# Optimization experiments

Measured on AMD Instinct MI355X. Metric: run time of the kernel, lower is better.

## Reference

```python
import jax, jax.numpy as jnp
import numpy as np

N_NODES = 100000
EMB = 256
HID = 64
N_REL = 5
N_EDGES = 3200000
BATCH = 16384


def _rgcn_conv(x, W, root, b, src, dst, etype):
    # PyG RGCNConv with mean aggregation per relation:
    # out_i = sum_r mean_{j in N_r(i)} x_j @ W_r + x_i @ root + b
    N = x.shape[0]
    R = W.shape[0]
    h = jnp.einsum('ni,rio->rno', x, W)          # [R, N, O] per-relation transforms
    m = h[etype, src]                            # [E, O] per-edge messages
    seg = dst * R + etype                        # combined (node, relation) segment id
    sums = jax.ops.segment_sum(m, seg, num_segments=N * R)
    cnt = jax.ops.segment_sum(jnp.ones((m.shape[0],), dtype=x.dtype), seg,
                              num_segments=N * R)
    mean = sums / jnp.maximum(cnt, 1.0)[:, None]
    agg = mean.reshape(N, R, -1).sum(axis=1)     # sum over relations
    return agg + x @ root + b


def _merge(x1, x2, w1, b1, w2, b2):
    x = jnp.concatenate([x1, x2], axis=1)
    h = jax.nn.relu(x @ w1 + b1)
    return h @ w2 + b2                           # [B, 1] logits


def setup_inputs() -> dict:
    key = jax.random.key(0)
    ks = jax.random.split(key, 16)
    d = {}
    d['bill_id'] = jax.random.randint(ks[0], (BATCH,), 0, N_NODES)
    d['user1_id'] = jax.random.randint(ks[1], (BATCH,), 0, N_NODES)
    d['user2_id'] = jax.random.randint(ks[2], (BATCH,), 0, N_NODES)
    d['edge_index'] = jax.random.randint(ks[3], (2, N_EDGES), 0, N_NODES)
    d['edge_type'] = jax.random.randint(ks[4], (N_EDGES,), 0, N_REL)
    # learned params (xavier-ish scaling); linear weights stored as [in, out]
    d['users_feature'] = jax.random.normal(ks[5], (N_NODES, EMB), jnp.float32) * 0.06
    d['W1'] = jax.random.normal(ks[6], (N_REL, EMB, HID), jnp.float32) * 0.08
    d['root1'] = jax.random.normal(ks[7], (EMB, HID), jnp.float32) * 0.08
    d['b1'] = jnp.zeros((HID,), jnp.float32)
    d['W2'] = jax.random.normal(ks[8], (N_REL, HID, HID), jnp.float32) * 0.12
    d['root2'] = jax.random.normal(ks[9], (HID, HID), jnp.float32) * 0.12
    d['b2'] = jnp.zeros((HID,), jnp.float32)
    d['mfc1_w'] = jax.random.normal(ks[10], (2 * HID, HID), jnp.float32) * 0.1
    d['mfc1_b'] = jnp.zeros((HID,), jnp.float32)
    d['mfc2_w'] = jax.random.normal(ks[11], (HID, 1), jnp.float32) * 0.17
    d['mfc2_b'] = jnp.zeros((1,), jnp.float32)
    return d


def reference(bill_id, user1_id, user2_id, edge_index, edge_type,
              users_feature, W1, root1, b1, W2, root2, b2,
              mfc1_w, mfc1_b, mfc2_w, mfc2_b):
    src, dst = edge_index[0], edge_index[1]
    x = jax.nn.relu(_rgcn_conv(users_feature, W1, root1, b1, src, dst, edge_type))
    nodes = _rgcn_conv(x, W2, root2, b2, src, dst, edge_type)  # [N, 64]
    bill = nodes[bill_id]
    u1 = nodes[user1_id]
    u2 = nodes[user2_id]
    pos = _merge(bill, u1, mfc1_w, mfc1_b, mfc2_w, mfc2_b)  # [B, 1]
    neg = _merge(bill, u2, mfc1_w, mfc1_b, mfc2_w, mfc2_b)
    z = jnp.concatenate([pos, neg], axis=0)
    t = jnp.concatenate([jnp.ones_like(pos), jnp.zeros_like(pos)], axis=0)
    # numerically stable BCE-with-logits, mean reduction
    bce = jnp.mean(jnp.maximum(z, 0.0) - z * t + jnp.log1p(jnp.exp(-jnp.abs(z))))
    pred = jnp.round(jax.nn.sigmoid(z))
    acc = jnp.mean((pred == t).astype(jnp.float32))
    return (bce, acc)
```

## Files before the change

kernel.cpp:

```cpp
#include <hip/hip_runtime.h>
#include <hip/hip_bf16.h>

#define N_NODES 100000
#define EMB 256
#define HID 64
#define N_REL 5
#define N_EDGES 3200000
#define BATCH 16384
#define NB 782
#define NWG1 256
#define CH 12500
#define LSEG 640
#define NSEG (N_NODES * N_REL)
#define NSLOT (3 * BATCH)
#define NSG 3072

typedef unsigned short u16;
typedef unsigned int u32;
typedef __attribute__((ext_vector_type(4))) float f32x4;
typedef __attribute__((ext_vector_type(8))) short short8;

__device__ __forceinline__ float bf2f(u16 u) {
    union { float f; u32 i; } v;
    v.i = ((u32)u) << 16;
    return v.f;
}
__device__ __forceinline__ u16 f2bf(float f) {
    union { float f; u32 i; } v;
    v.f = f;
    u32 r = v.i + 0x7fff + ((v.i >> 16) & 1);
    return (u16)(r >> 16);
}
__device__ __forceinline__ short8 pack8(float4 a, float4 b) {
    short8 r;
    r[0] = (short)f2bf(a.x); r[1] = (short)f2bf(a.y);
    r[2] = (short)f2bf(a.z); r[3] = (short)f2bf(a.w);
    r[4] = (short)f2bf(b.x); r[5] = (short)f2bf(b.y);
    r[6] = (short)f2bf(b.z); r[7] = (short)f2bf(b.w);
    return r;
}

__device__ __forceinline__ void gload_lds16(const void* g, void* l) {
    __builtin_amdgcn_global_load_lds(
        (const __attribute__((address_space(1))) unsigned int*)g,
        (__attribute__((address_space(3))) unsigned int*)l, 16, 0, 0);
}

__global__ __launch_bounds__(256) void bucket_hist(const int* __restrict__ dst,
                                                   int* __restrict__ hist) {
    __shared__ int hl[NB];
    const int tid = threadIdx.x;
    for (int i = tid; i < NB; i += 256) hl[i] = 0;
    __syncthreads();
    const int w = blockIdx.x;
    const int s = w * CH, e = s + CH;
    for (int i = s + tid; i < e; i += 256)
        atomicAdd(&hl[dst[i] >> 7], 1);
    __syncthreads();
    for (int i = tid; i < NB; i += 256) hist[w * NB + i] = hl[i];
}

__global__ void col_scan(int* __restrict__ hist, int* __restrict__ btot) {
    const int b = blockIdx.x;
    const int lane = threadIdx.x;
    int carry = 0;
    for (int c = 0; c < NWG1; c += 64) {
        int v = hist[(c + lane) * NB + b];
        int incl = v;
#pragma unroll
        for (int off = 1; off < 64; off <<= 1) {
            int t = __shfl_up(incl, off);
            if (lane >= off) incl += t;
        }
        hist[(c + lane) * NB + b] = carry + (incl - v);
        carry += __shfl(incl, 63);
    }
    if (lane == 0) btot[b] = carry;
}

__global__ void btot_scan(const int* __restrict__ btot, int* __restrict__ boffs,
                          int* __restrict__ offs) {
    const int lane = threadIdx.x;
    int carry = 0;
    for (int c = 0; c < NB; c += 64) {
        int v = (c + lane < NB) ? btot[c + lane] : 0;
        int incl = v;
#pragma unroll
        for (int off = 1; off < 64; off <<= 1) {
            int t = __shfl_up(incl, off);
            if (lane >= off) incl += t;
        }
        if (c + lane < NB) boffs[c + lane] = carry + (incl - v);
        carry += __shfl(incl, 63);
    }
    if (lane == 0) {
        boffs[NB] = N_EDGES;
        offs[NSEG] = N_EDGES;
    }
}

__global__ __launch_bounds__(256) void bucket_scatter(
        const int* __restrict__ src, const int* __restrict__ dst,
        const int* __restrict__ et, const int* __restrict__ base,
        const int* __restrict__ boffs, u32* __restrict__ bucketed) {
    __shared__ int cur[NB];
    const int tid = threadIdx.x;
    const int w = blockIdx.x;
    for (int i = tid; i < NB; i += 256) cur[i] = boffs[i] + base[w * NB + i];
    __syncthreads();
    const int s = w * CH, e = s + CH;
    for (int i = s + tid; i < e; i += 256) {
        int d = dst[i];
        int b = d >> 7;
        u32 key = (u32)src[i] | ((u32)((d & 127) * 5 + et[i]) << 17);
        int pos = atomicAdd(&cur[b], 1);
        bucketed[pos] = key;
    }
}

__global__ __launch_bounds__(256) void seg_sort(
        const u32* __restrict__ keys, const int* __restrict__ boffs,
        int* __restrict__ offs, u32* __restrict__ ssrc) {
    __shared__ int cntl[LSEG];
    __shared__ int cur[LSEG];
    const int tid = threadIdx.x;
    const int b = blockIdx.x;
    const int s = boffs[b], e = boffs[b + 1];

    for (int i = tid; i < LSEG; i += 256) cntl[i] = 0;
    __syncthreads();
    for (int i = s + tid; i < e; i += 256)
        atomicAdd(&cntl[keys[i] >> 17], 1);
    __syncthreads();

    if (tid < 64) {
        int carry = 0;
        for (int c = 0; c < LSEG; c += 64) {
            int v = cntl[c + tid];
            int incl = v;
#pragma unroll
            for (int off = 1; off < 64; off <<= 1) {
                int t = __shfl_up(incl, off);
                if (tid >= off) incl += t;
            }
            cur[c + tid] = carry + (incl - v);
            carry += __shfl(incl, 63);
        }
    }
    __syncthreads();

    const int segbase = b * LSEG;
    for (int i = tid; i < LSEG; i += 256)
        if (segbase + i < NSEG) offs[segbase + i] = s + cur[i];
    __syncthreads();

    for (int i = s + tid; i < e; i += 256) {
        u32 key = keys[i];
        int pos = s + atomicAdd(&cur[key >> 17], 1);
        ssrc[pos] = key & 0x1FFFF;
    }
}

__global__ void build_bt(const float* __restrict__ W, const float* __restrict__ root,
                         int K, u16* __restrict__ BT) {
    int idx = blockIdx.x * blockDim.x + threadIdx.x;
    if (idx >= 384 * K) return;
    int j = idx / K, k = idx - j * K;
    float v = (j < 320) ? W[((j >> 6) * K + k) * 64 + (j & 63)]
                        : root[k * 64 + (j & 63)];
    BT[idx] = f2bf(v);
}

template <int K, bool A_F32>
__global__ __launch_bounds__(512) void gemm384(
        const void* __restrict__ Av, const u16* __restrict__ BT,
        u16* __restrict__ C) {
    __shared__ __align__(16) u16 Al[128 * 64];
    __shared__ __align__(16) u16 Bl[384 * 64];
    const int tid  = threadIdx.x;
    const int lane = tid & 63;
    const int w    = tid >> 6;
    const int m0 = blockIdx.x * 128;
    const int wr = (w >> 2) * 64;
    const int wc = (w & 3) * 96;
    const int l15 = lane & 15;
    const int lg  = lane >> 4;

    f32x4 acc[4][6];
#pragma unroll
    for (int i = 0; i < 4; ++i)
#pragma unroll
        for (int j = 0; j < 6; ++j) {
            f32x4 z = {0.f, 0.f, 0.f, 0.f};
            acc[i][j] = z;
        }

    for (int k0 = 0; k0 < K; k0 += 64) {
#pragma unroll
        for (int j = 0; j < 6; ++j) {
            int c = (j * 8 + w) * 64 + lane;
            int row = c >> 3, sub = c & 7;
            gload_lds16(BT + (size_t)row * K + k0 + ((sub ^ (row & 7)) * 8),
                        &Bl[(j * 8 + w) * 512]);
        }
        if (A_F32) {
            const float* Af = (const float*)Av;
            int row = tid >> 2;
            int q0  = (tid & 3) * 2;
            int grow = min(m0 + row, N_NODES - 1);
            const float4* p = (const float4*)(Af + (size_t)grow * K + k0 + q0 * 8);
            float4 v0 = p[0], v1 = p[1], v2 = p[2], v3 = p[3];
            *(short8*)&Al[row * 64 + ((q0 ^ (row & 7)) * 8)]       = pack8(v0, v1);
            *(short8*)&Al[row * 64 + (((q0 + 1) ^ (row & 7)) * 8)] = pack8(v2, v3);
        } else {
            const u16* Ab = (const u16*)Av;
#pragma unroll
            for (int i = 0; i < 2; ++i) {
                int c = (i * 8 + w) * 64 + lane;
                int row = c >> 3, sub = c & 7;
                gload_lds16(Ab + (size_t)(m0 + row) * K + k0 + ((sub ^ (row & 7)) * 8),
                            &Al[(i * 8 + w) * 512]);
            }
        }
        __syncthreads();

#pragma unroll
        for (int kk = 0; kk < 64; kk += 32) {
            const int ch = (kk >> 3) + lg;
            short8 af[4], bf[6];
#pragma unroll
            for (int f = 0; f < 4; ++f) {
                int row = wr + f * 16 + l15;
                af[f] = *(const short8*)&Al[row * 64 + ((ch ^ (row & 7)) * 8)];
            }
#pragma unroll
            for (int f = 0; f < 6; ++f) {
                int col = wc + f * 16 + l15;
                bf[f] = *(const short8*)&Bl[col * 64 + ((ch ^ (col & 7)) * 8)];
            }
#pragma unroll
            for (int fm = 0; fm < 4; ++fm)
#pragma unroll
                for (int fn = 0; fn < 6; ++fn)
                    acc[fm][fn] = __builtin_amdgcn_mfma_f32_16x16x32_bf16(
                        bf[fn], af[fm], acc[fm][fn], 0, 0, 0);
        }
        __syncthreads();
    }

    char* Cst = (char*)Bl;
#pragma unroll
    for (int half = 0; half < 2; ++half) {
        if ((w >> 2) == half) {
#pragma unroll
            for (int fm = 0; fm < 4; ++fm) {
                int row_l = fm * 16 + l15;
#pragma unroll
                for (int fn = 0; fn < 6; ++fn) {
                    ushort4 p;
                    p.x = f2bf(acc[fm][fn][0]); p.y = f2bf(acc[fm][fn][1]);
                    p.z = f2bf(acc[fm][fn][2]); p.w = f2bf(acc[fm][fn][3]);
                    int colb  = (wc + fn * 16 + lg * 4) * 2;
                    int chunk = colb >> 4;
                    int addr  = row_l * 768 + (((chunk ^ (row_l & 7)) << 4) | (colb & 15));
                    *(ushort4*)(Cst + addr) = p;
                }
            }
        }
        __syncthreads();
#pragma unroll
        for (int it = 0; it < 6; ++it) {
            int idx = it * 512 + tid;
            int row_l = idx / 48;
            int chk = idx - row_l * 48;
            int r = m0 + half * 64 + row_l;
            if (r < N_NODES) {
                float4 v = *(const float4*)(Cst + row_l * 768 + ((chk ^ (row_l & 7)) << 4));
                *(float4*)(C + (size_t)r * 384 + chk * 8) = v;
            }
        }
        __syncthreads();
    }
}

template <bool RELU>
__global__ __launch_bounds__(256) void agg_rl(
        const u16* __restrict__ h, const u32* __restrict__ ssrc,
        const int* __restrict__ offs, const float* __restrict__ bias,
        u16* __restrict__ out) {
    const int lane = threadIdx.x & 63;
    const int d = (blockIdx.x * blockDim.x + threadIdx.x) >> 6;
    if (d >= N_NODES) return;

    const int o0 = offs[d * 5 + 0], o1 = offs[d * 5 + 1], o2 = offs[d * 5 + 2];
    const int o3 = offs[d * 5 + 3], o4 = offs[d * 5 + 4], o5 = offs[d * 5 + 5];
    const float i0 = 1.f / (float)max(o1 - o0, 1);
    const float i1 = 1.f / (float)max(o2 - o1, 1);
    const float i2 = 1.f / (float)max(o3 - o2, 1);
    const float i3 = 1.f / (float)max(o4 - o3, 1);
    const float i4 = 1.f / (float)max(o5 - o4, 1);

    const u16* hl = h + lane;
    float acc0 = bf2f(h[(size_t)d * 384 + 320 + lane]) + bias[lane];
    float acc1 = 0.f;

    for (int base = o0; base < o5; base += 64) {
        const int idx = base + lane;
        const u32 s = ssrc[min(idx, o5 - 1)];
        u32 reladd;
        float wv;
        if (idx < o1)      { reladd = 0;   wv = i0; }
        else if (idx < o2) { reladd = 64;  wv = i1; }
        else if (idx < o3) { reladd = 128; wv = i2; }
        else if (idx < o4) { reladd = 192; wv = i3; }
        else               { reladd = 256; wv = i4; }
        if (idx >= o5) wv = 0.f;
        const u32 voff = s * 384u + reladd;
        const int m = min(64, o5 - base);
        for (int j = 0; j < m; j += 8) {
#pragma unroll
            for (int jj = 0; jj < 8; jj += 2) {
                int  offa = __builtin_amdgcn_readlane((int)voff, j + jj);
                int  wa_i = __builtin_amdgcn_readlane((int)__float_as_uint(wv), j + jj);
                int  offb = __builtin_amdgcn_readlane((int)voff, j + jj + 1);
                int  wb_i = __builtin_amdgcn_readlane((int)__float_as_uint(wv), j + jj + 1);
                acc0 += bf2f(hl[(u32)offa]) * __uint_as_float((u32)wa_i);
                acc1 += bf2f(hl[(u32)offb]) * __uint_as_float((u32)wb_i);
            }
        }
    }
    float acc = acc0 + acc1;
    if (RELU) acc = fmaxf(acc, 0.f);
    out[(size_t)d * 64 + lane] = f2bf(acc);
}

__global__ __launch_bounds__(1024) void agg_mm2(
        const u16* __restrict__ x1, const u32* __restrict__ ssrc,
        const int* __restrict__ offs,
        const int* __restrict__ bill, const int* __restrict__ u1,
        const int* __restrict__ u2,
        const float* __restrict__ W2, const float* __restrict__ root2,
        const float* __restrict__ b2, u16* __restrict__ semb) {
    __shared__ __align__(16) u16 WT[64 * 392];
    __shared__ __align__(16) u16 Al[16 * 392];
    const int tid  = threadIdx.x;
    const int lane = tid & 63;
    const int wv   = tid >> 6;
    const int l15  = lane & 15;
    const int lg   = lane >> 4;

    for (int i = tid; i < 384 * 64; i += 1024) {
        int j = i >> 6, o = i & 63;
        float v = (j < 320) ? W2[i] : root2[i - 320 * 64];
        WT[o * 392 + j] = f2bf(v);
    }
    __syncthreads();

    const float b2v = b2[(wv & 3) * 16 + l15];

    for (int g = blockIdx.x; g < NSG; g += gridDim.x) {
        const int slot = g * 16 + wv;
        const int n = (slot < BATCH) ? bill[slot]
                    : (slot < 2 * BATCH) ? u1[slot - BATCH]
                    : u2[slot - 2 * BATCH];
        int o[6];
#pragma unroll
        for (int r = 0; r < 6; ++r) o[r] = offs[n * 5 + r];
        Al[wv * 392 + 320 + lane] = x1[(size_t)n * 64 + lane];

        float am[5];
#pragma unroll
        for (int r = 0; r < 5; ++r) am[r] = 0.f;

        const int o0 = o[0], o5 = o[5];
        for (int base = o0; base < o5; base += 64) {
            u32 voff = ssrc[min(base + lane, o5 - 1)] << 6;
#pragma unroll
            for (int r = 0; r < 5; ++r) {
                int jlo = max(o[r], base) - base;
                int jhi = min(o[r + 1], base + 64) - base;
                float s0 = 0.f, s1 = 0.f;
                int j = jlo;
                for (; j + 1 < jhi; j += 2) {
                    int oa = __builtin_amdgcn_readlane((int)voff, j);
                    int ob = __builtin_amdgcn_readlane((int)voff, j + 1);
                    s0 += bf2f(x1[(u32)oa + lane]);
                    s1 += bf2f(x1[(u32)ob + lane]);
                }
                if (j < jhi) {
                    int oa = __builtin_amdgcn_readlane((int)voff, j);
                    s0 += bf2f(x1[(u32)oa + lane]);
                }
                am[r] += s0 + s1;
            }
        }
#pragma unroll
        for (int r = 0; r < 5; ++r) {
            float inv = 1.f / (float)max(o[r + 1] - o[r], 1);
            Al[wv * 392 + r * 64 + lane] = f2bf(am[r] * inv);
        }
        __syncthreads();

        if (wv < 4) {
            f32x4 acc = {0.f, 0.f, 0.f, 0.f};
#pragma unroll
            for (int ks = 0; ks < 12; ++ks) {
                short8 af = *(const short8*)&Al[l15 * 392 + ks * 32 + lg * 8];
                short8 bf = *(const short8*)&WT[(wv * 16 + l15) * 392 + ks * 32 + lg * 8];
                acc = __builtin_amdgcn_mfma_f32_16x16x32_bf16(af, bf, acc, 0, 0, 0);
            }
            const int s0g = g * 16;
#pragma unroll
            for (int i = 0; i < 4; ++i)
                semb[(size_t)(s0g + lg * 4 + i) * 64 + wv * 16 + l15] =
                    f2bf(acc[i] + b2v);
        }
        __syncthreads();
    }
}

__global__ __launch_bounds__(256) void loss_kernel(
        const u16* __restrict__ semb,
        const float* __restrict__ w1, const float* __restrict__ b1,
        const float* __restrict__ w2, const float* __restrict__ b2,
        float* __restrict__ out) {
    __shared__ float Wl[128 * 64];
    __shared__ float red[2][4];
    for (int j = threadIdx.x; j < 128 * 16; j += 256)
        ((float4*)Wl)[j] = ((const float4*)w1)[j];
    __syncthreads();

    const int lane = threadIdx.x & 63;
    const int wv   = threadIdx.x >> 6;
    const int gw   = blockIdx.x * 4 + wv;
    const int nw   = gridDim.x * 4;

    const float bias1 = b1[lane];
    const float w2l   = w2[lane];
    const float bias2 = b2[0];

    float bce_acc = 0.f, corr_acc = 0.f;
    for (int s = gw; s < BATCH; s += nw) {
        const u16* xb  = semb + (size_t)s * 64;
        const u16* xu1 = semb + (size_t)(BATCH + s) * 64;
        const u16* xu2 = semb + (size_t)(2 * BATCH + s) * 64;
        float hb = bias1, h1 = 0.f, h2 = 0.f;
#pragma unroll 8
        for (int i = 0; i < 64; ++i) {
            float wb = Wl[i * 64 + lane];
            float wu = Wl[(64 + i) * 64 + lane];
            hb += bf2f(xb[i]) * wb;
            h1 += bf2f(xu1[i]) * wu;
            h2 += bf2f(xu2[i]) * wu;
        }
        float p1 = fmaxf(hb + h1, 0.f) * w2l;
        float p2 = fmaxf(hb + h2, 0.f) * w2l;
#pragma unroll
        for (int off = 32; off > 0; off >>= 1) {
            p1 += __shfl_down(p1, off);
            p2 += __shfl_down(p2, off);
        }
        if (lane == 0) {
            float z1 = p1 + bias2;
            float z2 = p2 + bias2;
            bce_acc += fmaxf(z1, 0.f) - z1 + log1pf(expf(-fabsf(z1)));
            bce_acc += fmaxf(z2, 0.f)      + log1pf(expf(-fabsf(z2)));
            corr_acc += (z1 > 0.f) ? 1.f : 0.f;
            corr_acc += (z2 > 0.f) ? 0.f : 1.f;
        }
    }
    if (lane == 0) { red[0][wv] = bce_acc; red[1][wv] = corr_acc; }
    __syncthreads();
    if (threadIdx.x == 0) {
        const float scale = 1.f / (2.f * BATCH);
        atomicAdd(&out[0], (red[0][0] + red[0][1] + red[0][2] + red[0][3]) * scale);
        atomicAdd(&out[1], (red[1][0] + red[1][1] + red[1][2] + red[1][3]) * scale);
    }
}

extern "C" void kernel_launch(void* const* d_in, const int* in_sizes, int n_in,
                              void* d_out, int out_size, void* d_ws, size_t ws_size,
                              hipStream_t stream) {
    const int*   bill  = (const int*)d_in[0];
    const int*   u1    = (const int*)d_in[1];
    const int*   u2    = (const int*)d_in[2];
    const int*   ei    = (const int*)d_in[3];
    const int*   et    = (const int*)d_in[4];
    const float* uf    = (const float*)d_in[5];
    const float* W1    = (const float*)d_in[6];
    const float* root1 = (const float*)d_in[7];
    const float* b1    = (const float*)d_in[8];
    const float* W2    = (const float*)d_in[9];
    const float* root2 = (const float*)d_in[10];
    const float* b2    = (const float*)d_in[11];
    const float* m1w   = (const float*)d_in[12];
    const float* m1b   = (const float*)d_in[13];
    const float* m2w   = (const float*)d_in[14];
    const float* m2b   = (const float*)d_in[15];
    float* out = (float*)d_out;

    char* ws = (char*)d_ws;
    u16* h_all    = (u16*)(ws);
    u16* semb     = (u16*)(ws);
    u32* ssrc     = (u32*)(ws + 76800000);
    u32* bucketed = (u32*)(ws + 89600000);
    u16* xbuf     = (u16*)(ws + 89600000);
    int* hist     = (int*)(ws + 102400000);
    int* btot     = (int*)(ws + 103200768);
    int* boffs    = (int*)(ws + 103203896);
    int* offs     = (int*)(ws + 103207040);
    u16* BT1      = (u16*)(ws + 105207056);
    if (ws_size < 105452816) return;

    const int* src = ei;
    const int* dst = ei + N_EDGES;

    hipMemsetAsync(d_out, 0, 2 * sizeof(float), stream);

    bucket_hist<<<NWG1, 256, 0, stream>>>(dst, hist);
    col_scan<<<NB, 64, 0, stream>>>(hist, btot);
    btot_scan<<<1, 64, 0, stream>>>(btot, boffs, offs);
    bucket_scatter<<<NWG1, 256, 0, stream>>>(src, dst, et, hist, boffs, bucketed);
    seg_sort<<<NB, 256, 0, stream>>>(bucketed, boffs, offs, ssrc);

    build_bt<<<(384 * EMB + 255) / 256, 256, 0, stream>>>(W1, root1, EMB, BT1);

    gemm384<EMB, true><<<782, 512, 0, stream>>>(uf, BT1, h_all);
    agg_rl<true><<<25000, 256, 0, stream>>>(h_all, ssrc, offs, b1, xbuf);

    agg_mm2<<<1024, 1024, 0, stream>>>(xbuf, ssrc, offs, bill, u1, u2,
                                       W2, root2, b2, semb);

    loss_kernel<<<1024, 256, 0, stream>>>(semb, m1w, m1b, m2w, m2b, out);
}
```

Before: 326.9 us.

## Split layer-1 GEMM into two N-tiles with 256-thread blocks

The layer-1 384-wide GEMM now uses a 2D grid where each 256-thread block computes a 128x192 output tile instead of 128x384 with 512 threads. This halves shared memory per block and allows up to four blocks per CU, aiming for better occupancy and more workgroups to spread across CUs. The cost is that each A tile (fp32 input rows) is now loaded and converted twice, once per N half. The unused bf16-A path is also removed.

```diff
diff --git a/kernel.cpp b/kernel.cpp
--- a/kernel.cpp
+++ b/kernel.cpp
@@ -171,18 +171,19 @@
     BT[idx] = f2bf(v);
 }
 
-template <int K, bool A_F32>
-__global__ __launch_bounds__(512) void gemm384(
-        const void* __restrict__ Av, const u16* __restrict__ BT,
+template <int K>
+__global__ __launch_bounds__(256, 4) void gemm384(
+        const float* __restrict__ Af, const u16* __restrict__ BT,
         u16* __restrict__ C) {
     __shared__ __align__(16) u16 Al[128 * 64];
-    __shared__ __align__(16) u16 Bl[384 * 64];
+    __shared__ __align__(16) u16 Bl[192 * 64];
     const int tid  = threadIdx.x;
     const int lane = tid & 63;
     const int w    = tid >> 6;
-    const int m0 = blockIdx.x * 128;
-    const int wr = (w >> 2) * 64;
-    const int wc = (w & 3) * 96;
+    const int m0  = blockIdx.x * 128;
+    const int n0  = blockIdx.y * 192;
+    const int wr = (w >> 1) * 64;
+    const int wc = (w & 1) * 96;
     const int l15 = lane & 15;
     const int lg  = lane >> 4;
 
@@ -198,29 +199,22 @@
     for (int k0 = 0; k0 < K; k0 += 64) {
 #pragma unroll
         for (int j = 0; j < 6; ++j) {
-            int c = (j * 8 + w) * 64 + lane;
+            int c = (j * 4 + w) * 64 + lane;
             int row = c >> 3, sub = c & 7;
-            gload_lds16(BT + (size_t)row * K + k0 + ((sub ^ (row & 7)) * 8),
-                        &Bl[(j * 8 + w) * 512]);
-        }
-        if (A_F32) {
-            const float* Af = (const float*)Av;
-            int row = tid >> 2;
-            int q0  = (tid & 3) * 2;
+            gload_lds16(BT + (size_t)(n0 + row) * K + k0 + ((sub ^ (row & 7)) * 8),
+                        &Bl[(j * 4 + w) * 512]);
+        }
+        {
+            int row = tid >> 1;
+            int q0  = (tid & 1) * 4;
             int grow = min(m0 + row, N_NODES - 1);
             const float4* p = (const float4*)(Af + (size_t)grow * K + k0 + q0 * 8);
             float4 v0 = p[0], v1 = p[1], v2 = p[2], v3 = p[3];
-            *(short8*)&Al[row * 64 + ((q0 ^ (row & 7)) * 8)]       = pack8(v0, v1);
+            float4 v4 = p[4], v5 = p[5], v6 = p[6], v7 = p[7];
+            *(short8*)&Al[row * 64 + (((q0 + 0) ^ (row & 7)) * 8)] = pack8(v0, v1);
             *(short8*)&Al[row * 64 + (((q0 + 1) ^ (row & 7)) * 8)] = pack8(v2, v3);
-        } else {
-            const u16* Ab = (const u16*)Av;
-#pragma unroll
-            for (int i = 0; i < 2; ++i) {
-                int c = (i * 8 + w) * 64 + lane;
-                int row = c >> 3, sub = c & 7;
-                gload_lds16(Ab + (size_t)(m0 + row) * K + k0 + ((sub ^ (row & 7)) * 8),
-                            &Al[(i * 8 + w) * 512]);
-            }
+            *(short8*)&Al[row * 64 + (((q0 + 2) ^ (row & 7)) * 8)] = pack8(v4, v5);
+            *(short8*)&Al[row * 64 + (((q0 + 3) ^ (row & 7)) * 8)] = pack8(v6, v7);
         }
         __syncthreads();
 
@@ -251,7 +245,7 @@
     char* Cst = (char*)Bl;
 #pragma unroll
     for (int half = 0; half < 2; ++half) {
-        if ((w >> 2) == half) {
+        if ((w >> 1) == half) {
 #pragma unroll
             for (int fm = 0; fm < 4; ++fm) {
                 int row_l = fm * 16 + l15;
@@ -262,7 +256,7 @@
                     p.z = f2bf(acc[fm][fn][2]); p.w = f2bf(acc[fm][fn][3]);
                     int colb  = (wc + fn * 16 + lg * 4) * 2;
                     int chunk = colb >> 4;
-                    int addr  = row_l * 768 + (((chunk ^ (row_l & 7)) << 4) | (colb & 15));
+                    int addr  = row_l * 384 + (((chunk ^ (row_l & 7)) << 4) | (colb & 15));
                     *(ushort4*)(Cst + addr) = p;
                 }
             }
@@ -270,13 +264,13 @@
         __syncthreads();
 #pragma unroll
         for (int it = 0; it < 6; ++it) {
-            int idx = it * 512 + tid;
-            int row_l = idx / 48;
-            int chk = idx - row_l * 48;
+            int idx = it * 256 + tid;
+            int row_l = idx / 24;
+            int chk = idx - row_l * 24;
             int r = m0 + half * 64 + row_l;
             if (r < N_NODES) {
-                float4 v = *(const float4*)(Cst + row_l * 768 + ((chk ^ (row_l & 7)) << 4));
-                *(float4*)(C + (size_t)r * 384 + chk * 8) = v;
+                float4 v = *(const float4*)(Cst + row_l * 384 + ((chk ^ (row_l & 7)) << 4));
+                *(float4*)(C + (size_t)r * 384 + n0 + chk * 8) = v;
             }
         }
         __syncthreads();
@@ -525,7 +519,7 @@
 
     build_bt<<<(384 * EMB + 255) / 256, 256, 0, stream>>>(W1, root1, EMB, BT1);
 
-    gemm384<EMB, true><<<782, 512, 0, stream>>>(uf, BT1, h_all);
+    gemm384<EMB><<<dim3(782, 2), 256, 0, stream>>>(uf, BT1, h_all);
     agg_rl<true><<<25000, 256, 0, stream>>>(h_all, ssrc, offs, b1, xbuf);
 
     agg_mm2<<<1024, 1024, 0, stream>>>(xbuf, ssrc, offs, bill, u1, u2,
```

After: 494.9 us. 1.51x slower.

## Double-buffer LDS tiles in first-layer GEMM to overlap loads with MFMA

Applied to the files above, without the earlier changes.

Replaces the single-buffered 64-wide K tile GEMM with a double-buffered 32-wide K tile version. It prefetches the next B tile through direct-to-LDS loads and the next A tile into registers while MFMAs run on the current buffer, which halves the barriers per tile. The aim is to hide global load latency behind compute. The trade-off is twice as many K iterations, a different swizzle pattern, and unchanged total LDS use.

```diff
diff --git a/kernel.cpp b/kernel.cpp
--- a/kernel.cpp
+++ b/kernel.cpp
@@ -171,12 +171,12 @@
     BT[idx] = f2bf(v);
 }
 
-template <int K, bool A_F32>
-__global__ __launch_bounds__(512) void gemm384(
-        const void* __restrict__ Av, const u16* __restrict__ BT,
+template <int K>
+__global__ __launch_bounds__(512) void gemm_db(
+        const float* __restrict__ Af, const u16* __restrict__ BT,
         u16* __restrict__ C) {
-    __shared__ __align__(16) u16 Al[128 * 64];
-    __shared__ __align__(16) u16 Bl[384 * 64];
+    __shared__ __align__(16) u16 Al[2][128 * 32];
+    __shared__ __align__(16) u16 Bl[2][384 * 32];
     const int tid  = threadIdx.x;
     const int lane = tid & 63;
     const int w    = tid >> 6;
@@ -186,6 +186,10 @@
     const int l15 = lane & 15;
     const int lg  = lane >> 4;
 
+    const int arow = tid >> 2;
+    const int aq   = tid & 3;
+    const int agrow = min(m0 + arow, N_NODES - 1);
+
     f32x4 acc[4][6];
 #pragma unroll
     for (int i = 0; i < 4; ++i)
@@ -195,48 +199,47 @@
             acc[i][j] = z;
         }
 
-    for (int k0 = 0; k0 < K; k0 += 64) {
-#pragma unroll
-        for (int j = 0; j < 6; ++j) {
+    {
+#pragma unroll
+        for (int j = 0; j < 3; ++j) {
             int c = (j * 8 + w) * 64 + lane;
-            int row = c >> 3, sub = c & 7;
-            gload_lds16(BT + (size_t)row * K + k0 + ((sub ^ (row & 7)) * 8),
-                        &Bl[(j * 8 + w) * 512]);
-        }
-        if (A_F32) {
-            const float* Af = (const float*)Av;
-            int row = tid >> 2;
-            int q0  = (tid & 3) * 2;
-            int grow = min(m0 + row, N_NODES - 1);
-            const float4* p = (const float4*)(Af + (size_t)grow * K + k0 + q0 * 8);
-            float4 v0 = p[0], v1 = p[1], v2 = p[2], v3 = p[3];
-            *(short8*)&Al[row * 64 + ((q0 ^ (row & 7)) * 8)]       = pack8(v0, v1);
-            *(short8*)&Al[row * 64 + (((q0 + 1) ^ (row & 7)) * 8)] = pack8(v2, v3);
-        } else {
-            const u16* Ab = (const u16*)Av;
-#pragma unroll
-            for (int i = 0; i < 2; ++i) {
-                int c = (i * 8 + w) * 64 + lane;
-                int row = c >> 3, sub = c & 7;
-                gload_lds16(Ab + (size_t)(m0 + row) * K + k0 + ((sub ^ (row & 7)) * 8),
-                            &Al[(i * 8 + w) * 512]);
-            }
-        }
-        __syncthreads();
-
-#pragma unroll
-        for (int kk = 0; kk < 64; kk += 32) {
-            const int ch = (kk >> 3) + lg;
+            int row = c >> 2, sub = c & 3;
+            gload_lds16(BT + (size_t)row * K + ((sub ^ ((row >> 1) & 3)) * 8),
+                        &Bl[0][(j * 8 + w) * 512]);
+        }
+        const float4* p = (const float4*)(Af + (size_t)agrow * K + aq * 8);
+        float4 v0 = p[0], v1 = p[1];
+        *(short8*)&Al[0][arow * 32 + ((aq ^ ((arow >> 1) & 3)) * 8)] = pack8(v0, v1);
+    }
+    __syncthreads();
+
+    for (int k0 = 0; k0 < K; k0 += 32) {
+        const int cur = (k0 >> 5) & 1;
+        const bool more = (k0 + 32) < K;
+        float4 va, vb;
+        if (more) {
+#pragma unroll
+            for (int j = 0; j < 3; ++j) {
+                int c = (j * 8 + w) * 64 + lane;
+                int row = c >> 2, sub = c & 3;
+                gload_lds16(BT + (size_t)row * K + k0 + 32 + ((sub ^ ((row >> 1) & 3)) * 8),
+                            &Bl[cur ^ 1][(j * 8 + w) * 512]);
+            }
+            const float4* p = (const float4*)(Af + (size_t)agrow * K + k0 + 32 + aq * 8);
+            va = p[0]; vb = p[1];
+        }
+
+        {
             short8 af[4], bf[6];
 #pragma unroll
             for (int f = 0; f < 4; ++f) {
                 int row = wr + f * 16 + l15;
-                af[f] = *(const short8*)&Al[row * 64 + ((ch ^ (row & 7)) * 8)];
+                af[f] = *(const short8*)&Al[cur][row * 32 + ((lg ^ ((row >> 1) & 3)) * 8)];
             }
 #pragma unroll
             for (int f = 0; f < 6; ++f) {
                 int col = wc + f * 16 + l15;
-                bf[f] = *(const short8*)&Bl[col * 64 + ((ch ^ (col & 7)) * 8)];
+                bf[f] = *(const short8*)&Bl[cur][col * 32 + ((lg ^ ((col >> 1) & 3)) * 8)];
             }
 #pragma unroll
             for (int fm = 0; fm < 4; ++fm)
@@ -244,6 +247,10 @@
                 for (int fn = 0; fn < 6; ++fn)
                     acc[fm][fn] = __builtin_amdgcn_mfma_f32_16x16x32_bf16(
                         bf[fn], af[fm], acc[fm][fn], 0, 0, 0);
+        }
+
+        if (more) {
+            *(short8*)&Al[cur ^ 1][arow * 32 + ((aq ^ ((arow >> 1) & 3)) * 8)] = pack8(va, vb);
         }
         __syncthreads();
     }
@@ -525,7 +532,7 @@
 
     build_bt<<<(384 * EMB + 255) / 256, 256, 0, stream>>>(W1, root1, EMB, BT1);
 
-    gemm384<EMB, true><<<782, 512, 0, stream>>>(uf, BT1, h_all);
+    gemm_db<EMB><<<782, 512, 0, stream>>>(uf, BT1, h_all);
     agg_rl<true><<<25000, 256, 0, stream>>>(h_all, ssrc, offs, b1, xbuf);
 
     agg_mm2<<<1024, 1024, 0, stream>>>(xbuf, ssrc, offs, bill, u1, u2,
```

Measured after the change: 326.8 us (median of 3 runs). About the same (-0.0%).
